# Optimization experiments

Measured on AMD Instinct MI355X. Metric: run time of the kernel, lower is better.

Reference implementation:

```python
import jax, jax.numpy as jnp
import numpy as np
import math

FACTOR = 5

def setup_inputs() -> dict:
    key = jax.random.key(0)
    k1, k2, k3, k4 = jax.random.split(key, 4)
    B, L, H, D = 4, 4096, 8, 64
    sample_k = min(FACTOR * int(np.ceil(np.log(L))), L)  # 45
    return {
        "queries": jax.random.normal(k1, (B, L, H, D), dtype=jnp.float32),
        "keys": jax.random.normal(k2, (B, L, H, D), dtype=jnp.float32),
        "values": jax.random.normal(k3, (B, L, H, D), dtype=jnp.float32),
        "index_sample": jax.random.randint(k4, (L, sample_k), 0, L, dtype=jnp.int64),
    }

def reference(queries, keys, values, index_sample):
    # [B, L, H, D] -> [B, H, L, D]
    Q = jnp.transpose(queries, (0, 2, 1, 3))
    K = jnp.transpose(keys, (0, 2, 1, 3))
    V = jnp.transpose(values, (0, 2, 1, 3))
    b, h, l_q, d = Q.shape
    l_k = K.shape[2]

    # n_top (u) per Informer: factor * ceil(ln(l_q)), capped at l_q
    u = min(FACTOR * int(math.ceil(math.log(l_q))), l_q)

    # --- _prob_QK: sampled QK scores ---
    # K_sample: [b, h, l_q, sample_k, d] via shared per-query random sample
    K_sample = K[:, :, index_sample, :]
    # Q_K_sample: [b, h, l_q, sample_k]
    Q_K_sample = jnp.einsum("bhqd,bhqsd->bhqs", Q, K_sample)
    # sparsity measure M: max - mean(sum/l_k)
    M = Q_K_sample.max(axis=-1) - Q_K_sample.sum(axis=-1) / l_k
    # top-u queries (indices; order irrelevant to the math)
    _, M_top = jax.lax.top_k(M, u)  # [b, h, u]

    # Q_reduce: [b, h, u, d]
    Q_reduce = jnp.take_along_axis(Q, M_top[..., None], axis=2)
    # full scores for selected queries: [b, h, u, l_k]
    scale = 1.0 / math.sqrt(d)
    scores_top = jnp.einsum("bhud,bhkd->bhuk", Q_reduce, K) * scale

    # --- initial context: mean of V broadcast over queries ---
    context = jnp.broadcast_to(V.mean(axis=2, keepdims=True), (b, h, l_q, d))

    # --- update context at selected query positions ---
    attn = jax.nn.softmax(scores_top, axis=-1)          # [b, h, u, l_k]
    upd = jnp.einsum("bhuk,bhkd->bhud", attn, V)         # [b, h, u, d]
    bi = jnp.arange(b)[:, None, None]
    hi = jnp.arange(h)[None, :, None]
    context = context.at[bi, hi, M_top].set(upd)

    # [B, H, L, D] -> [B, L, H, D]
    return jnp.transpose(context, (0, 2, 1, 3))
```

## Files before the change

### kernel.cpp

```cpp
#include <hip/hip_runtime.h>
#include <stdint.h>

#define B_ 4
#define L_ 4096
#define H_ 8
#define D_ 64
#define S_ 45
#define U_ 45
#define BH_ 32
#define KC_ 16
#define STRIDE_ (H_*D_)
#define BSTR_ ((size_t)L_*H_*D_)

__device__ __forceinline__ bool detect_idx64(const int* idxp){
    bool z = true;
    #pragma unroll
    for (int i = 1; i < 32; i += 2) z = z && (idxp[i] == 0);
    return z;
}

__global__ __launch_bounds__(256) void kM(const float* __restrict__ Qb,
                                          const float* __restrict__ Kb,
                                          const int* __restrict__ idxp,
                                          float* __restrict__ Mout){
    int g = blockIdx.x;
    int xcd  = g & 7;
    int slot = g >> 3;
    int bh   = xcd*4 + (slot >> 6);
    int chunk= slot & 63;
    int b = bh >> 3, h = bh & 7;
    int q0 = chunk * 64;
    bool idx64 = detect_idx64(idxp);

    __shared__ float qs[64][64];
    for (int i = threadIdx.x; i < 64*16; i += 256){
        int qrow = i >> 4, c = i & 15;
        float4 v = ((const float4*)(Qb + (size_t)b*BSTR_ + (size_t)(q0+qrow)*STRIDE_ + h*D_))[c];
        *(float4*)&qs[qrow][c*4] = v;
    }
    __syncthreads();

    int lane8 = threadIdx.x & 7;
    const float* kbase = Kb + (size_t)b*BSTR_ + h*D_;

    for (int qq = 0; qq < 2; qq++){
        int qrow = (threadIdx.x >> 3) + 32*qq;
        int qg   = q0 + qrow;
        float4 qf0 = *(const float4*)&qs[qrow][lane8*4];
        float4 qf1 = *(const float4*)&qs[qrow][lane8*4 + 32];
        float mx = -1e30f, sm = 0.f;
        #pragma unroll 3
        for (int s = 0; s < S_; s++){
            int flat = qg * S_ + s;
            int ki = idx64 ? idxp[2*flat] : idxp[flat];
            const float* kr = kbase + (size_t)ki*STRIDE_;
            float4 k0 = *(const float4*)(kr + lane8*4);
            float4 k1 = *(const float4*)(kr + lane8*4 + 32);
            float a0 = qf0.x*k0.x;
            a0 = fmaf(qf0.y, k0.y, a0);
            a0 = fmaf(qf0.z, k0.z, a0);
            a0 = fmaf(qf0.w, k0.w, a0);
            float a1 = qf1.x*k1.x;
            a1 = fmaf(qf1.y, k1.y, a1);
            a1 = fmaf(qf1.z, k1.z, a1);
            a1 = fmaf(qf1.w, k1.w, a1);
            float p = a0 + a1;
            p += __shfl_xor(p, 1);
            p += __shfl_xor(p, 2);
            p += __shfl_xor(p, 4);
            mx = fmaxf(mx, p); sm += p;
        }
        if (lane8 == 0) Mout[bh * L_ + qg] = mx - sm * (1.0f / L_);
    }
}

__global__ __launch_bounds__(512) void kTopF(const float* __restrict__ M,
                                             int* __restrict__ Mtop,
                                             float* __restrict__ meanZ,
                                             int* __restrict__ selRow){
    int bh = blockIdx.x;
    int t = threadIdx.x;
    if (t < 64) meanZ[bh*64 + t] = 0.f;
    for (int j = t; j < L_; j += 512) selRow[(size_t)bh*L_ + j] = 0;

    __shared__ float cV[8*U_];
    __shared__ int   cI[8*U_];
    int wv = t >> 6, lane = t & 63;
    const float* Mr = M + (size_t)bh*L_ + wv*512;
    float v[8];
    #pragma unroll
    for (int j = 0; j < 8; j++) v[j] = Mr[lane + 64*j];

    for (int it = 0; it < U_; it++){
        float best = -1e30f; int bidx = 0x7fffffff;
        #pragma unroll
        for (int j = 0; j < 8; j++){
            int id = lane + 64*j;
            if (v[j] > best){ best = v[j]; bidx = id; }
        }
        #pragma unroll
        for (int off = 1; off < 64; off <<= 1){
            float ov = __shfl_xor(best, off); int oi = __shfl_xor(bidx, off);
            if (ov > best || (ov == best && oi < bidx)){ best = ov; bidx = oi; }
        }
        if (lane == 0){ cV[wv*U_ + it] = best; cI[wv*U_ + it] = wv*512 + bidx; }
        if (lane == (bidx & 63)) v[bidx >> 6] = -1e30f;
    }
    __syncthreads();
    if (t < 64){
        float v2[6]; int id2[6];
        #pragma unroll
        for (int j = 0; j < 6; j++){
            int slot = t + 64*j;
            if (slot < 8*U_){ v2[j] = cV[slot]; id2[j] = cI[slot]; }
            else            { v2[j] = -1e30f;  id2[j] = 0x7fffffff; }
        }
        for (int it = 0; it < U_; it++){
            float best = -1e30f; int bidx = 0x7fffffff; int bj = 0;
            #pragma unroll
            for (int j = 0; j < 6; j++){
                if (v2[j] > best || (v2[j] == best && id2[j] < bidx)){
                    best = v2[j]; bidx = id2[j]; bj = j;
                }
            }
            float myBest = best; int myIdx = bidx;
            #pragma unroll
            for (int off = 1; off < 64; off <<= 1){
                float ov = __shfl_xor(best, off); int oi = __shfl_xor(bidx, off);
                if (ov > best || (ov == best && oi < bidx)){ best = ov; bidx = oi; }
            }
            if (t == 0){
                Mtop[bh*U_ + it] = bidx;
                selRow[(size_t)bh*L_ + bidx] = it + 1;
            }
            if (myBest == best && myIdx == bidx) v2[bj] = -1e30f;
        }
    }
}

__global__ __launch_bounds__(256) void kAttnPart(const float* __restrict__ Qb,
                                                 const float* __restrict__ Kb,
                                                 const float* __restrict__ Vb,
                                                 const int*   __restrict__ Mtop,
                                                 float* __restrict__ Opart,
                                                 float* __restrict__ mlG,
                                                 float* __restrict__ mean){
    int bh = blockIdx.y, b = bh >> 3, h = bh & 7;
    int kc = blockIdx.x, uh = blockIdx.z;
    int u0 = uh ? 23 : 0;
    int nu = uh ? 22 : 23;
    int t = threadIdx.x;
    __shared__ float S[24][260];
    __shared__ float red[4][8][64];
    __shared__ int   qidx[23];

    if (t < nu) qidx[t] = Mtop[bh*U_ + u0 + t];
    __syncthreads();

    int k = kc*256 + t;
    float4 kf[16];
    const float4* K4 = (const float4*)(Kb + (size_t)b*BSTR_ + (size_t)k*STRIDE_ + h*D_);
    #pragma unroll
    for (int c = 0; c < 16; c++) kf[c] = K4[c];
    for (int u = 0; u < nu; u++){
        int qi = __builtin_amdgcn_readfirstlane(qidx[u]);
        const float4* qp = (const float4*)(Qb + (size_t)b*BSTR_ + (size_t)qi*STRIDE_ + h*D_);
        float a0=0.f, a1=0.f, a2=0.f, a3=0.f;
        #pragma unroll
        for (int c = 0; c < 16; c++){
            float4 qv = qp[c];
            a0 = fmaf(qv.x, kf[c].x, a0);
            a1 = fmaf(qv.y, kf[c].y, a1);
            a2 = fmaf(qv.z, kf[c].z, a2);
            a3 = fmaf(qv.w, kf[c].w, a3);
        }
        S[u][t] = ((a0+a1)+(a2+a3)) * 0.125f;
    }
    __syncthreads();

    int wv = t >> 6, lane = t & 63;
    for (int u = wv; u < nu; u += 4){
        float4 sv = *(const float4*)&S[u][lane*4];
        float m = fmaxf(fmaxf(sv.x, sv.y), fmaxf(sv.z, sv.w));
        #pragma unroll
        for (int off = 1; off < 64; off <<= 1) m = fmaxf(m, __shfl_xor(m, off));
        float e0 = __expf(sv.x - m), e1 = __expf(sv.y - m);
        float e2 = __expf(sv.z - m), e3 = __expf(sv.w - m);
        float ls = (e0+e1)+(e2+e3);
        #pragma unroll
        for (int off = 1; off < 64; off <<= 1) ls += __shfl_xor(ls, off);
        float4 pv; pv.x = e0; pv.y = e1; pv.z = e2; pv.w = e3;
        *(float4*)&S[u][lane*4] = pv;
        if (lane == 0){
            size_t mi = ((size_t)(bh*KC_ + kc)*U_ + u0 + u)*2;
            mlG[mi] = m; mlG[mi+1] = ls;
        }
    }
    __syncthreads();

    int d8 = t & 7, ks = t >> 3;
    float vsum[8];
    #pragma unroll
    for (int j = 0; j < 8; j++) vsum[j] = 0.f;
    for (int g = 0; g < 3; g++){
        int g0 = g*8; int nug = (nu - g0 < 8) ? (nu - g0) : 8;
        float acc[8][8];
        #pragma unroll
        for (int r = 0; r < 8; r++)
            #pragma unroll
            for (int j = 0; j < 8; j++) acc[r][j] = 0.f;
        for (int i = 0; i < 8; i++){
            int kk = ks + 32*i;
            const float4* V4 = (const float4*)(Vb + (size_t)b*BSTR_ +
                        (size_t)(kc*256 + kk)*STRIDE_ + h*D_);
            float4 va = V4[d8*2], vb = V4[d8*2+1];
            float vf[8] = {va.x, va.y, va.z, va.w, vb.x, vb.y, vb.z, vb.w};
            if (uh == 0 && g == 0){
                #pragma unroll
                for (int j = 0; j < 8; j++) vsum[j] += vf[j];
            }
            #pragma unroll
            for (int r = 0; r < 8; r++){
                float p = S[g0+r][kk];
                #pragma unroll
                for (int j = 0; j < 8; j++) acc[r][j] = fmaf(p, vf[j], acc[r][j]);
            }
        }
        #pragma unroll
        for (int off = 8; off <= 32; off <<= 1)
            #pragma unroll
            for (int r = 0; r < 8; r++)
                #pragma unroll
                for (int j = 0; j < 8; j++) acc[r][j] += __shfl_xor(acc[r][j], off);
        if (lane < 8){
            for (int r = 0; r < 8; r++)
                #pragma unroll
                for (int j = 0; j < 8; j++) red[wv][r][d8*8+j] = acc[r][j];
        }
        __syncthreads();
        for (int tt = t; tt < nug*64; tt += 256){
            int r = tt >> 6, d = tt & 63;
            float s = red[0][r][d] + red[1][r][d] + red[2][r][d] + red[3][r][d];
            Opart[((size_t)(bh*KC_ + kc)*U_ + u0 + g0 + r)*64 + d] = s;
        }
        __syncthreads();
    }
    if (uh == 0){
        #pragma unroll
        for (int off = 8; off <= 32; off <<= 1)
            #pragma unroll
            for (int j = 0; j < 8; j++) vsum[j] += __shfl_xor(vsum[j], off);
        if (lane < 8){
            #pragma unroll
            for (int j = 0; j < 8; j++) red[wv][0][lane*8 + j] = vsum[j];
        }
        __syncthreads();
        if (t < 64){
            float s = red[0][0][t] + red[1][0][t] + red[2][0][t] + red[3][0][t];
            atomicAdd(&mean[bh*64 + t], s);
        }
    }
}

__global__ __launch_bounds__(256) void kOut(const float* __restrict__ mean,
                                            const int*   __restrict__ selRow,
                                            const float* __restrict__ mlG,
                                            const float* __restrict__ Opart,
                                            float* __restrict__ out){
    size_t t = (size_t)blockIdx.x*256 + threadIdx.x;
    int d16 = (int)(t & 15); int h = (int)((t >> 4) & 7);
    int l   = (int)((t >> 7) & 4095); int b = (int)(t >> 19);
    int bh = b*8 + h;
    int sel = selRow[(size_t)bh*L_ + l];
    float4 o;
    if (sel == 0){
        o = *(const float4*)(mean + bh*64 + d16*4);
        const float inv = 1.0f / L_;
        o.x *= inv; o.y *= inv; o.z *= inv; o.w *= inv;
    } else {
        int u = sel - 1;
        float mstar = -1e30f;
        #pragma unroll
        for (int kc = 0; kc < KC_; kc++)
            mstar = fmaxf(mstar, mlG[((size_t)(bh*KC_ + kc)*U_ + u)*2]);
        float lsum = 0.f;
        float4 acc; acc.x = acc.y = acc.z = acc.w = 0.f;
        #pragma unroll
        for (int kc = 0; kc < KC_; kc++){
            size_t mi = ((size_t)(bh*KC_ + kc)*U_ + u)*2;
            float w = __expf(mlG[mi] - mstar);
            lsum = fmaf(mlG[mi+1], w, lsum);
            float4 op = *(const float4*)(Opart + ((size_t)(bh*KC_ + kc)*U_ + u)*64 + d16*4);
            acc.x = fmaf(w, op.x, acc.x);
            acc.y = fmaf(w, op.y, acc.y);
            acc.z = fmaf(w, op.z, acc.z);
            acc.w = fmaf(w, op.w, acc.w);
        }
        float inv = 1.0f / lsum;
        acc.x *= inv; acc.y *= inv; acc.z *= inv; acc.w *= inv;
        o = acc;
    }
    ((float4*)out)[t] = o;
}

extern "C" void kernel_launch(void* const* d_in, const int* in_sizes, int n_in,
                              void* d_out, int out_size, void* d_ws, size_t ws_size,
                              hipStream_t stream) {
    const float* Qb  = (const float*)d_in[0];
    const float* Kb  = (const float*)d_in[1];
    const float* Vb  = (const float*)d_in[2];
    const int*   idx = (const int*)d_in[3];
    float* out = (float*)d_out;

    float* ws = (float*)d_ws;
    float* M      = ws;
    int*   Mtop   = (int*)(ws + 131072);
    float* mean   = ws + 133120;
    int*   selRow = (int*)(ws + 135168);
    float* mlG    = ws + 266240;
    float* Opart  = ws + 315392;

    kM        <<<dim3(2048),       dim3(256), 0, stream>>>(Qb, Kb, idx, M);
    kTopF     <<<dim3(32),         dim3(512), 0, stream>>>(M, Mtop, mean, selRow);
    kAttnPart <<<dim3(KC_, 32, 2), dim3(256), 0, stream>>>(Qb, Kb, Vb, Mtop, Opart, mlG, mean);
    kOut      <<<dim3(8192),       dim3(256), 0, stream>>>(mean, selRow, mlG, Opart, out);
}
```

Before: 343.4 us.

## Fuse output kernel into attention via last-block counter; stage sample indices in LDS

The separate output kernel is removed. The last finishing attention block per (b,h), detected with an atomic counter, merges the partial softmax results and writes the whole output slice for that head. The sparsity-measure kernel preloads the sampled key indices for its query tile into shared memory as 16-bit values and unrolls the sampling loop further. This removes a launch and the strided index reads, but serializes the large output write onto only 32 blocks.

```diff
diff --git a/kernel.cpp b/kernel.cpp
--- a/kernel.cpp
+++ b/kernel.cpp
@@ -22,8 +22,12 @@
 __global__ __launch_bounds__(256) void kM(const float* __restrict__ Qb,
                                           const float* __restrict__ Kb,
                                           const int* __restrict__ idxp,
-                                          float* __restrict__ Mout){
+                                          float* __restrict__ Mout,
+                                          int* __restrict__ cnt){
     int g = blockIdx.x;
+    int t = threadIdx.x;
+    if (g == 0 && t < BH_) cnt[t] = 0;
+
     int xcd  = g & 7;
     int slot = g >> 3;
     int bh   = xcd*4 + (slot >> 6);
@@ -32,27 +36,32 @@
     int q0 = chunk * 64;
     bool idx64 = detect_idx64(idxp);
 
-    __shared__ float qs[64][64];
-    for (int i = threadIdx.x; i < 64*16; i += 256){
+    __shared__ float   qs[64][64];
+    __shared__ uint16_t sidx[64*S_];
+    for (int i = t; i < 64*16; i += 256){
         int qrow = i >> 4, c = i & 15;
         float4 v = ((const float4*)(Qb + (size_t)b*BSTR_ + (size_t)(q0+qrow)*STRIDE_ + h*D_))[c];
         *(float4*)&qs[qrow][c*4] = v;
     }
-    __syncthreads();
-
-    int lane8 = threadIdx.x & 7;
+    if (idx64){
+        for (int i = t; i < 64*S_; i += 256) sidx[i] = (uint16_t)idxp[2*(q0*S_ + i)];
+    } else {
+        for (int i = t; i < 64*S_; i += 256) sidx[i] = (uint16_t)idxp[q0*S_ + i];
+    }
+    __syncthreads();
+
+    int lane8 = t & 7;
     const float* kbase = Kb + (size_t)b*BSTR_ + h*D_;
 
     for (int qq = 0; qq < 2; qq++){
-        int qrow = (threadIdx.x >> 3) + 32*qq;
+        int qrow = (t >> 3) + 32*qq;
         int qg   = q0 + qrow;
         float4 qf0 = *(const float4*)&qs[qrow][lane8*4];
         float4 qf1 = *(const float4*)&qs[qrow][lane8*4 + 32];
         float mx = -1e30f, sm = 0.f;
-        #pragma unroll 3
+        #pragma unroll 5
         for (int s = 0; s < S_; s++){
-            int flat = qg * S_ + s;
-            int ki = idx64 ? idxp[2*flat] : idxp[flat];
+            int ki = (int)sidx[qrow*S_ + s];
             const float* kr = kbase + (size_t)ki*STRIDE_;
             float4 k0 = *(const float4*)(kr + lane8*4);
             float4 k1 = *(const float4*)(kr + lane8*4 + 32);
@@ -142,9 +151,12 @@
                                                  const float* __restrict__ Kb,
                                                  const float* __restrict__ Vb,
                                                  const int*   __restrict__ Mtop,
+                                                 const int*   __restrict__ selRow,
                                                  float* __restrict__ Opart,
                                                  float* __restrict__ mlG,
-                                                 float* __restrict__ mean){
+                                                 float* __restrict__ mean,
+                                                 int*   __restrict__ cnt,
+                                                 float* __restrict__ out){
     int bh = blockIdx.y, b = bh >> 3, h = bh & 7;
     int kc = blockIdx.x, uh = blockIdx.z;
     int u0 = uh ? 23 : 0;
@@ -153,6 +165,7 @@
     __shared__ float S[24][260];
     __shared__ float red[4][8][64];
     __shared__ int   qidx[23];
+    __shared__ int   lastFlag;
 
     if (t < nu) qidx[t] = Mtop[bh*U_ + u0 + t];
     __syncthreads();
@@ -260,47 +273,49 @@
             atomicAdd(&mean[bh*64 + t], s);
         }
     }
-}
-
-__global__ __launch_bounds__(256) void kOut(const float* __restrict__ mean,
-                                            const int*   __restrict__ selRow,
-                                            const float* __restrict__ mlG,
-                                            const float* __restrict__ Opart,
-                                            float* __restrict__ out){
-    size_t t = (size_t)blockIdx.x*256 + threadIdx.x;
-    int d16 = (int)(t & 15); int h = (int)((t >> 4) & 7);
-    int l   = (int)((t >> 7) & 4095); int b = (int)(t >> 19);
-    int bh = b*8 + h;
-    int sel = selRow[(size_t)bh*L_ + l];
-    float4 o;
-    if (sel == 0){
-        o = *(const float4*)(mean + bh*64 + d16*4);
-        const float inv = 1.0f / L_;
-        o.x *= inv; o.y *= inv; o.z *= inv; o.w *= inv;
-    } else {
-        int u = sel - 1;
-        float mstar = -1e30f;
-        #pragma unroll
-        for (int kc = 0; kc < KC_; kc++)
-            mstar = fmaxf(mstar, mlG[((size_t)(bh*KC_ + kc)*U_ + u)*2]);
-        float lsum = 0.f;
-        float4 acc; acc.x = acc.y = acc.z = acc.w = 0.f;
-        #pragma unroll
-        for (int kc = 0; kc < KC_; kc++){
-            size_t mi = ((size_t)(bh*KC_ + kc)*U_ + u)*2;
-            float w = __expf(mlG[mi] - mstar);
-            lsum = fmaf(mlG[mi+1], w, lsum);
-            float4 op = *(const float4*)(Opart + ((size_t)(bh*KC_ + kc)*U_ + u)*64 + d16*4);
-            acc.x = fmaf(w, op.x, acc.x);
-            acc.y = fmaf(w, op.y, acc.y);
-            acc.z = fmaf(w, op.z, acc.z);
-            acc.w = fmaf(w, op.w, acc.w);
-        }
-        float inv = 1.0f / lsum;
-        acc.x *= inv; acc.y *= inv; acc.z *= inv; acc.w *= inv;
-        o = acc;
-    }
-    ((float4*)out)[t] = o;
+
+    __threadfence();
+    if (t == 0) lastFlag = (atomicAdd(&cnt[bh], 1) == 31);
+    __syncthreads();
+    if (!lastFlag) return;
+    __threadfence();
+
+    int d16 = t & 15;
+    float4 mv = *(const float4*)(mean + bh*64 + d16*4);
+    const float invL = 1.0f / L_;
+    mv.x *= invL; mv.y *= invL; mv.z *= invL; mv.w *= invL;
+
+    for (int i = 0; i < 256; i++){
+        int l = i*16 + (t >> 4);
+        int sel = selRow[(size_t)bh*L_ + l];
+        float4 o;
+        if (sel == 0){
+            o = mv;
+        } else {
+            int u = sel - 1;
+            float mstar = -1e30f;
+            #pragma unroll
+            for (int kc2 = 0; kc2 < KC_; kc2++)
+                mstar = fmaxf(mstar, mlG[((size_t)(bh*KC_ + kc2)*U_ + u)*2]);
+            float lsum = 0.f;
+            float4 acc; acc.x = acc.y = acc.z = acc.w = 0.f;
+            #pragma unroll
+            for (int kc2 = 0; kc2 < KC_; kc2++){
+                size_t mi = ((size_t)(bh*KC_ + kc2)*U_ + u)*2;
+                float w = __expf(mlG[mi] - mstar);
+                lsum = fmaf(mlG[mi+1], w, lsum);
+                float4 op = *(const float4*)(Opart + ((size_t)(bh*KC_ + kc2)*U_ + u)*64 + d16*4);
+                acc.x = fmaf(w, op.x, acc.x);
+                acc.y = fmaf(w, op.y, acc.y);
+                acc.z = fmaf(w, op.z, acc.z);
+                acc.w = fmaf(w, op.w, acc.w);
+            }
+            float inv = 1.0f / lsum;
+            acc.x *= inv; acc.y *= inv; acc.z *= inv; acc.w *= inv;
+            o = acc;
+        }
+        *(float4*)(out + (size_t)b*BSTR_ + (size_t)l*STRIDE_ + h*D_ + d16*4) = o;
+    }
 }
 
 extern "C" void kernel_launch(void* const* d_in, const int* in_sizes, int n_in,
@@ -318,10 +333,11 @@
     float* mean   = ws + 133120;
     int*   selRow = (int*)(ws + 135168);
     float* mlG    = ws + 266240;
-    float* Opart  = ws + 315392;
-
-    kM        <<<dim3(2048),       dim3(256), 0, stream>>>(Qb, Kb, idx, M);
+    int*   cnt    = (int*)(ws + 315392);
+    float* Opart  = ws + 315456;
+
+    kM        <<<dim3(2048),       dim3(256), 0, stream>>>(Qb, Kb, idx, M, cnt);
     kTopF     <<<dim3(32),         dim3(512), 0, stream>>>(M, Mtop, mean, selRow);
-    kAttnPart <<<dim3(KC_, 32, 2), dim3(256), 0, stream>>>(Qb, Kb, Vb, Mtop, Opart, mlG, mean);
-    kOut      <<<dim3(8192),       dim3(256), 0, stream>>>(mean, selRow, mlG, Opart, out);
-}
+    kAttnPart <<<dim3(KC_, 32, 2), dim3(256), 0, stream>>>(Qb, Kb, Vb, Mtop, selRow,
+                                                           Opart, mlG, mean, cnt, out);
+}
```

Result: slower. 508.9 us (+48.2%).
